# Kernel tuning notes

Hardware: AMD Instinct MI355X
Metric: run time of the kernel (lower is better)

## Reference

```python
import jax, jax.numpy as jnp
import numpy as np

N_VERT, D = 100000, 128
N_EDGE, K, R = 20000, 8, 4


def setup_inputs() -> dict:
    key = jax.random.key(0)
    ks = jax.random.split(key, 16)
    s = 0.05
    return {
        'feats': jax.random.normal(ks[0], (N_VERT, D), dtype=jnp.float32),
        'edge_members': jax.random.randint(ks[1], (N_EDGE, K), 0, N_VERT),
        'adj_members': jax.random.randint(ks[2], (N_EDGE, R, K), 0, N_VERT),
        'ids': jnp.arange(N_EDGE),
        'epoch': 10,
        # VertexConv params (Linear(d,1) each)
        'wq': jax.random.normal(ks[3], (D, 1)) * s, 'bq': jnp.zeros((1,)),
        'wk': jax.random.normal(ks[4], (D, 1)) * s, 'bk': jnp.zeros((1,)),
        'wv': jax.random.normal(ks[5], (D, 1)) * s, 'bv': jnp.zeros((1,)),
        # EdgeConv MLP: Linear(d, d//4) -> ReLU -> Linear(d//4, 1)
        'W1': jax.random.normal(ks[6], (D, D // 4)) * s, 'b1': jnp.zeros((D // 4,)),
        'W2': jax.random.normal(ks[7], (D // 4, 1)) * s, 'b2': jnp.zeros((1,)),
        # final classifier Linear(d, 2)
        'Wfc': jax.random.normal(ks[8], (D, 2)) * s, 'bfc': jnp.zeros((2,)),
    }


def _vertex_conv(feats, members, wq, bq, wk, bk, wv, bv):
    # members: [E, K] vertex indices; aggregates each hyperedge's vertices into one feature.
    f = feats[members]                         # [E,K,d] irregular gather
    q = f @ wq + bq                            # [E,K,1]
    k = f @ wk + bk                            # [E,K,1]
    v = f @ wv + bv                            # [E,K,1]
    # score[e,j,l] = q[e,j]*k[e,l]; original softmaxes over the K-1 "other" vertices (l != j)
    S = q * jnp.swapaxes(k, -1, -2)            # [E,K,K]
    S = jnp.where(jnp.eye(members.shape[-1], dtype=bool), -jnp.inf, S)
    a = jax.nn.softmax(S, axis=-1)             # [E,K,K]
    di = jnp.tanh(jnp.einsum('ejl,elo->ejo', a, v))  # [E,K,1] per-vertex scalar gate
    return (di * f).sum(axis=1)                # [E,d]


def reference(feats, edge_members, adj_members, ids, epoch,
              wq, bq, wk, bk, wv, bv, W1, b1, W2, b2, Wfc, bfc):
    n = edge_members.shape[0]
    # epoch >= wu_e(=0): hyperedge feature from edge_dict
    xn = _vertex_conv(feats, edge_members, wq, bq, wk, bk, wv, bv)   # [N,d]
    # epoch >= wu_a(=5): hyperedge features from each vertex's adjacent edges
    xe = _vertex_conv(feats, adj_members.reshape(n * R, K),
                      wq, bq, wk, bk, wv, bv).reshape(n, R, -1)       # [N,R,d]
    ft = jnp.concatenate([xn[:, None, :], xe], axis=1)                # [N,1+R,d]
    # EdgeConv: attention over the 1+R candidate hyperedge feats
    sc = jax.nn.relu(ft @ W1 + b1) @ W2 + b2                          # [N,1+R,1]
    a = jax.nn.softmax(sc, axis=1)
    h = (a * ft).sum(axis=1)                                          # [N,d]
    # dropout in eval mode (identity), then sigmoid(Linear(d,2))
    return jax.nn.sigmoid(h @ Wfc + bfc)                              # [N,2]
```

## Files before the change

kernel.cpp:

```cpp
#include <hip/hip_runtime.h>
#include <math.h>

#define KK 8
#define DD 128
#define RR 4
#define NG 5
#define HID 32
#define NC 40
#define NSLOT 48

typedef __attribute__((ext_vector_type(8))) short short8_t;
typedef __attribute__((ext_vector_type(4))) float f32x4_t;

__device__ __forceinline__ unsigned short f2bf(float x) {
    unsigned int u = __float_as_uint(x);
    unsigned int r = (u + 0x7FFFu + ((u >> 16) & 1u)) >> 16;
    return (unsigned short)r;
}
__device__ __forceinline__ float bf2f(unsigned short u) {
    return __uint_as_float((unsigned int)u << 16);
}

__global__ __launch_bounds__(256) void proj_mfma(
    const float* __restrict__ feats, int n_vert, int n_tg,
    const float* __restrict__ wq, const float* __restrict__ wk,
    const float* __restrict__ wv, const float* __restrict__ Wfc,
    const float* __restrict__ W1,
    const float* __restrict__ bq, const float* __restrict__ bk,
    const float* __restrict__ bv,
    unsigned short* __restrict__ proj)
{
    __shared__ short Bsh[12 * 64 * 8];

    const int t = threadIdx.x;
    const int wave = t >> 6, lane = t & 63;
    const int row = lane & 15;
    const int kg  = lane >> 4;

    #pragma unroll
    for (int q = 0; q < 3; ++q) {
        const int p = t + q * 256;
        const int ntks = p >> 6, plane = p & 63;
        const int nt = ntks >> 2, ks = ntks & 3;
        const int n  = nt * 16 + (plane & 15);
        const int k0 = ks * 32 + (plane >> 4) * 8;
        short8_t v;
        #pragma unroll
        for (int j = 0; j < 8; ++j) {
            const int k = k0 + j;
            float val;
            if      (n == 0) val = wq[k];
            else if (n == 1) val = wk[k];
            else if (n == 2) val = wv[k];
            else if (n == 3) val = Wfc[2 * k];
            else if (n == 4) val = Wfc[2 * k + 1];
            else if (n < 37) val = W1[k * HID + (n - 5)];
            else             val = 0.f;
            v[j] = (short)f2bf(val);
        }
        *(short8_t*)&Bsh[p * 8] = v;
    }

    const float bq0 = bq[0], bk0 = bk[0], bv0 = bv[0];
    __syncthreads();

    for (int tg = blockIdx.x; tg < n_tg; tg += gridDim.x) {
        const int mbase = (tg * 4 + wave) * 16;
        if (mbase >= n_vert) continue;

        long long arow = (long long)(mbase + row);
        if (arow >= n_vert) arow = n_vert - 1;
        const float* ar = &feats[arow * DD + kg * 8];
        float4 araw[8];
        #pragma unroll
        for (int ks = 0; ks < 4; ++ks) {
            araw[2 * ks]     = *(const float4*)&ar[ks * 32];
            araw[2 * ks + 1] = *(const float4*)&ar[ks * 32 + 4];
        }

        short8_t afrag[4];
        #pragma unroll
        for (int ks = 0; ks < 4; ++ks) {
            const float4 x0 = araw[2 * ks], x1 = araw[2 * ks + 1];
            short8_t a;
            a[0] = (short)f2bf(x0.x); a[1] = (short)f2bf(x0.y);
            a[2] = (short)f2bf(x0.z); a[3] = (short)f2bf(x0.w);
            a[4] = (short)f2bf(x1.x); a[5] = (short)f2bf(x1.y);
            a[6] = (short)f2bf(x1.z); a[7] = (short)f2bf(x1.w);
            afrag[ks] = a;
        }

        #pragma unroll
        for (int nt = 0; nt < 3; ++nt) {
            f32x4_t acc = {0.f, 0.f, 0.f, 0.f};
            #pragma unroll
            for (int ks = 0; ks < 4; ++ks) {
                const short8_t b = *(const short8_t*)&Bsh[((nt * 4 + ks) * 64 + lane) * 8];
                acc = __builtin_amdgcn_mfma_f32_16x16x32_bf16(afrag[ks], b, acc, 0, 0, 0);
            }
            const int col = nt * 16 + row;
            if (col < 37) {
                const int slot = (col < 5) ? col : (col + 3);
                float badd = 0.f;
                if      (col == 0) badd = bq0;
                else if (col == 1) badd = bk0;
                else if (col == 2) badd = bv0;
                #pragma unroll
                for (int r = 0; r < 4; ++r) {
                    const int vr = mbase + kg * 4 + r;
                    if (vr < n_vert)
                        proj[(long long)vr * NSLOT + slot] = f2bf(acc[r] + badd);
                }
            }
        }
    }
}

__global__ __launch_bounds__(256) void edge_fused(
    const int* __restrict__ edge_members,
    const int* __restrict__ adj_members,
    const unsigned short* __restrict__ proj,
    const float* __restrict__ b1, const float* __restrict__ W2,
    const float* __restrict__ b2, const float* __restrict__ bfc,
    float* __restrict__ out, int n_edge)
{
    __shared__ int   vidS[4][NG * KK];
    __shared__ float diS [4][NG * KK];
    __shared__ float ftfcS[4][NG][2];
    __shared__ float scS [4][NG];

    const int t = threadIdx.x;
    const int w = t >> 6;
    const int lane = t & 63;
    const int e = blockIdx.x * 4 + w;
    if (e >= n_edge) return;

    const int g = lane >> 3;
    const int j = lane & 7;
    const bool act = lane < NG * KK;

    int vid = 0;
    if (act) vid = (g == 0) ? edge_members[e * KK + j]
                            : adj_members[((e * RR) + (g - 1)) * KK + j];

    const uint4 qpu = *(const uint4*)&proj[(long long)vid * NSLOT];
    const float qv  = bf2f((unsigned short)(qpu.x & 0xFFFFu));
    const float kv  = bf2f((unsigned short)(qpu.x >> 16));
    const float vv  = bf2f((unsigned short)(qpu.y & 0xFFFFu));
    const float pf0 = bf2f((unsigned short)(qpu.y >> 16));
    const float pf1 = bf2f((unsigned short)(qpu.z & 0xFFFFu));

    float k8[KK], v8[KK];
    #pragma unroll
    for (int r = 0; r < KK; ++r) {
        k8[r] = __shfl(kv, (g << 3) + r);
        v8[r] = __shfl(vv, (g << 3) + r);
    }

    float mx = -1e30f;
    float s[KK];
    #pragma unroll
    for (int r = 0; r < KK; ++r) {
        s[r] = qv * k8[r];
        if (r != j) mx = fmaxf(mx, s[r]);
    }
    float den = 0.f, num = 0.f;
    #pragma unroll
    for (int r = 0; r < KK; ++r) {
        if (r == j) continue;
        const float ex = expf(s[r] - mx);
        den += ex;
        num += ex * v8[r];
    }
    const float di = tanhf(num / den);

    float px = di * pf0, py = di * pf1;
    #pragma unroll
    for (int mm = 4; mm >= 1; mm >>= 1) {
        px += __shfl_xor(px, mm);
        py += __shfl_xor(py, mm);
    }
    if (act) {
        vidS[w][lane] = vid;
        diS[w][lane]  = di;
        if (j == 0) { ftfcS[w][g][0] = px; ftfcS[w][g][1] = py; }
    }
    asm volatile("s_waitcnt lgkmcnt(0)" ::: "memory");

    const int m = lane & 31;
    const int h = lane >> 5;
    const float b1m = b1[m];
    const float w2m = W2[m];

    float dr2[3][KK];
    float pv2[3][KK];
    #pragma unroll
    for (int p = 0; p < 3; ++p) {
        const int grp = (p << 1) | h;
        if (grp < NG) {
            #pragma unroll
            for (int r = 0; r < KK; ++r) {
                const int vr = vidS[w][grp * KK + r];
                dr2[p][r] = diS[w][grp * KK + r];
                pv2[p][r] = bf2f(proj[(long long)vr * NSLOT + 8 + m]);
            }
        }
    }
    #pragma unroll
    for (int p = 0; p < 3; ++p) {
        const int grp = (p << 1) | h;
        if (grp < NG) {
            float acc = 0.f;
            #pragma unroll
            for (int r = 0; r < KK; ++r) acc += dr2[p][r] * pv2[p][r];
            float hid = fmaxf(acc + b1m, 0.f) * w2m;
            #pragma unroll
            for (int mm = 16; mm >= 1; mm >>= 1) hid += __shfl_xor(hid, mm);
            if (m == 0) scS[w][grp] = hid + b2[0];
        }
    }
    asm volatile("s_waitcnt lgkmcnt(0)" ::: "memory");

    if (lane < 2) {
        float sc0[NG];
        float m5 = -1e30f;
        #pragma unroll
        for (int gg = 0; gg < NG; ++gg) { sc0[gg] = scS[w][gg]; m5 = fmaxf(m5, sc0[gg]); }
        float ssum = 0.f;
        #pragma unroll
        for (int gg = 0; gg < NG; ++gg) { sc0[gg] = expf(sc0[gg] - m5); ssum += sc0[gg]; }
        const float inv = 1.f / ssum;
        float hc = 0.f;
        #pragma unroll
        for (int gg = 0; gg < NG; ++gg) hc += sc0[gg] * inv * ftfcS[w][gg][lane];
        const float z = hc + bfc[lane];
        out[e * 2 + lane] = 1.f / (1.f + expf(-z));
    }
}

extern "C" void kernel_launch(void* const* d_in, const int* in_sizes, int n_in,
                              void* d_out, int out_size, void* d_ws, size_t ws_size,
                              hipStream_t stream) {
    const float* feats        = (const float*)d_in[0];
    const int*   edge_members = (const int*)  d_in[1];
    const int*   adj_members  = (const int*)  d_in[2];
    const float* wq  = (const float*)d_in[5];
    const float* bq  = (const float*)d_in[6];
    const float* wk  = (const float*)d_in[7];
    const float* bk  = (const float*)d_in[8];
    const float* wv  = (const float*)d_in[9];
    const float* bv  = (const float*)d_in[10];
    const float* W1  = (const float*)d_in[11];
    const float* b1  = (const float*)d_in[12];
    const float* W2  = (const float*)d_in[13];
    const float* b2  = (const float*)d_in[14];
    const float* Wfc = (const float*)d_in[15];
    const float* bfc = (const float*)d_in[16];
    float* out = (float*)d_out;

    const int n_vert = in_sizes[0] / DD;
    const int n_edge = in_sizes[1] / KK;

    unsigned short* proj = (unsigned short*)d_ws;

    const int n_mtiles = (n_vert + 15) / 16;
    const int n_tg = (n_mtiles + 3) / 4;
    const int grid = (n_tg < 640) ? n_tg : 640;

    proj_mfma<<<grid, 256, 0, stream>>>(
        feats, n_vert, n_tg, wq, wk, wv, Wfc, W1, bq, bk, bv, proj);

    edge_fused<<<(n_edge + 3) / 4, 256, 0, stream>>>(
        edge_members, adj_members, proj, b1, W2, b2, bfc, out, n_edge);
}
```

Baseline: 41.97 us.

## Prefetch next feats tile in projection loop and drop LDS in edge kernel

The projection kernel now double-buffers its feature rows in registers, loading the next tile while converting and running MFMAs on the current one. The grid is resized so each block handles about two tiles. The edge kernel replaces shared-memory staging of vertex ids, gates and scores with wave shuffles, and issues the W1-hidden gathers early so they overlap the softmax math. This adds register pressure and extra shuffles in exchange for hiding global-load latency and removing LDS round trips.

```diff
diff --git a/kernel.cpp b/kernel.cpp
--- a/kernel.cpp
+++ b/kernel.cpp
@@ -6,7 +6,6 @@
 #define RR 4
 #define NG 5
 #define HID 32
-#define NC 40
 #define NSLOT 48
 
 typedef __attribute__((ext_vector_type(8))) short short8_t;
@@ -64,24 +63,42 @@
     const float bq0 = bq[0], bk0 = bk[0], bv0 = bv[0];
     __syncthreads();
 
-    for (int tg = blockIdx.x; tg < n_tg; tg += gridDim.x) {
-        const int mbase = (tg * 4 + wave) * 16;
-        if (mbase >= n_vert) continue;
-
-        long long arow = (long long)(mbase + row);
+    const int stride = gridDim.x;
+    int tg = blockIdx.x;
+    if (tg >= n_tg) return;
+
+    float4 cur[8];
+    {
+        long long arow = (long long)(tg * 4 + wave) * 16 + row;
         if (arow >= n_vert) arow = n_vert - 1;
         const float* ar = &feats[arow * DD + kg * 8];
-        float4 araw[8];
         #pragma unroll
         for (int ks = 0; ks < 4; ++ks) {
-            araw[2 * ks]     = *(const float4*)&ar[ks * 32];
-            araw[2 * ks + 1] = *(const float4*)&ar[ks * 32 + 4];
-        }
-
+            cur[2 * ks]     = *(const float4*)&ar[ks * 32];
+            cur[2 * ks + 1] = *(const float4*)&ar[ks * 32 + 4];
+        }
+    }
+
+    for (;;) {
+        const int tgn = tg + stride;
+        const bool more = (tgn < n_tg);
+        float4 nxt[8];
+        if (more) {
+            long long arow = (long long)(tgn * 4 + wave) * 16 + row;
+            if (arow >= n_vert) arow = n_vert - 1;
+            const float* ar = &feats[arow * DD + kg * 8];
+            #pragma unroll
+            for (int ks = 0; ks < 4; ++ks) {
+                nxt[2 * ks]     = *(const float4*)&ar[ks * 32];
+                nxt[2 * ks + 1] = *(const float4*)&ar[ks * 32 + 4];
+            }
+        }
+
+        const int mbase = (tg * 4 + wave) * 16;
         short8_t afrag[4];
         #pragma unroll
         for (int ks = 0; ks < 4; ++ks) {
-            const float4 x0 = araw[2 * ks], x1 = araw[2 * ks + 1];
+            const float4 x0 = cur[2 * ks], x1 = cur[2 * ks + 1];
             short8_t a;
             a[0] = (short)f2bf(x0.x); a[1] = (short)f2bf(x0.y);
             a[2] = (short)f2bf(x0.z); a[3] = (short)f2bf(x0.w);
@@ -89,7 +106,6 @@
             a[6] = (short)f2bf(x1.z); a[7] = (short)f2bf(x1.w);
             afrag[ks] = a;
         }
-
         #pragma unroll
         for (int nt = 0; nt < 3; ++nt) {
             f32x4_t acc = {0.f, 0.f, 0.f, 0.f};
@@ -113,6 +129,11 @@
                 }
             }
         }
+
+        if (!more) break;
+        #pragma unroll
+        for (int i = 0; i < 8; ++i) cur[i] = nxt[i];
+        tg = tgn;
     }
 }
 
@@ -124,11 +145,6 @@
     const float* __restrict__ b2, const float* __restrict__ bfc,
     float* __restrict__ out, int n_edge)
 {
-    __shared__ int   vidS[4][NG * KK];
-    __shared__ float diS [4][NG * KK];
-    __shared__ float ftfcS[4][NG][2];
-    __shared__ float scS [4][NG];
-
     const int t = threadIdx.x;
     const int w = t >> 6;
     const int lane = t & 63;
@@ -138,12 +154,27 @@
     const int g = lane >> 3;
     const int j = lane & 7;
     const bool act = lane < NG * KK;
+    const int m = lane & 31;
+    const int h = lane >> 5;
 
     int vid = 0;
     if (act) vid = (g == 0) ? edge_members[e * KK + j]
                             : adj_members[((e * RR) + (g - 1)) * KK + j];
 
     const uint4 qpu = *(const uint4*)&proj[(long long)vid * NSLOT];
+
+    float pv2[3][KK];
+    #pragma unroll
+    for (int p = 0; p < 3; ++p) {
+        const int grp = (p << 1) | h;
+        const int gsrc = (grp < NG) ? grp : 0;
+        #pragma unroll
+        for (int r = 0; r < KK; ++r) {
+            const int vr = __shfl(vid, gsrc * KK + r);
+            pv2[p][r] = bf2f(proj[(long long)vr * NSLOT + 8 + m]);
+        }
+    }
+
     const float qv  = bf2f((unsigned short)(qpu.x & 0xFFFFu));
     const float kv  = bf2f((unsigned short)(qpu.x >> 16));
     const float vv  = bf2f((unsigned short)(qpu.y & 0xFFFFu));
@@ -156,7 +187,6 @@
         k8[r] = __shfl(kv, (g << 3) + r);
         v8[r] = __shfl(vv, (g << 3) + r);
     }
-
     float mx = -1e30f;
     float s[KK];
     #pragma unroll
@@ -180,60 +210,46 @@
         px += __shfl_xor(px, mm);
         py += __shfl_xor(py, mm);
     }
-    if (act) {
-        vidS[w][lane] = vid;
-        diS[w][lane]  = di;
-        if (j == 0) { ftfcS[w][g][0] = px; ftfcS[w][g][1] = py; }
-    }
-    asm volatile("s_waitcnt lgkmcnt(0)" ::: "memory");
-
-    const int m = lane & 31;
-    const int h = lane >> 5;
+
     const float b1m = b1[m];
     const float w2m = W2[m];
-
-    float dr2[3][KK];
-    float pv2[3][KK];
+    float scr[3];
     #pragma unroll
     for (int p = 0; p < 3; ++p) {
         const int grp = (p << 1) | h;
-        if (grp < NG) {
-            #pragma unroll
-            for (int r = 0; r < KK; ++r) {
-                const int vr = vidS[w][grp * KK + r];
-                dr2[p][r] = diS[w][grp * KK + r];
-                pv2[p][r] = bf2f(proj[(long long)vr * NSLOT + 8 + m]);
-            }
-        }
-    }
-    #pragma unroll
-    for (int p = 0; p < 3; ++p) {
-        const int grp = (p << 1) | h;
-        if (grp < NG) {
-            float acc = 0.f;
-            #pragma unroll
-            for (int r = 0; r < KK; ++r) acc += dr2[p][r] * pv2[p][r];
-            float hid = fmaxf(acc + b1m, 0.f) * w2m;
-            #pragma unroll
-            for (int mm = 16; mm >= 1; mm >>= 1) hid += __shfl_xor(hid, mm);
-            if (m == 0) scS[w][grp] = hid + b2[0];
-        }
-    }
-    asm volatile("s_waitcnt lgkmcnt(0)" ::: "memory");
-
+        const int gsrc = (grp < NG) ? grp : 0;
+        float acc = 0.f;
+        #pragma unroll
+        for (int r = 0; r < KK; ++r)
+            acc += __shfl(di, gsrc * KK + r) * pv2[p][r];
+        float hid = fmaxf(acc + b1m, 0.f) * w2m;
+        #pragma unroll
+        for (int mm = 16; mm >= 1; mm >>= 1) hid += __shfl_xor(hid, mm);
+        scr[p] = hid;
+    }
+
+    float sc5[NG], fx5[NG], fy5[NG];
+    #pragma unroll
+    for (int gg = 0; gg < NG; ++gg) {
+        sc5[gg] = __shfl(scr[gg >> 1], (gg & 1) * 32) + b2[0];
+        fx5[gg] = __shfl(px, gg * 8);
+        fy5[gg] = __shfl(py, gg * 8);
+    }
+
+    float m5 = sc5[0];
+    #pragma unroll
+    for (int gg = 1; gg < NG; ++gg) m5 = fmaxf(m5, sc5[gg]);
+    float ssum = 0.f, h0 = 0.f, h1 = 0.f;
+    #pragma unroll
+    for (int gg = 0; gg < NG; ++gg) {
+        const float a = expf(sc5[gg] - m5);
+        ssum += a;
+        h0 += a * fx5[gg];
+        h1 += a * fy5[gg];
+    }
+    const float inv = 1.f / ssum;
     if (lane < 2) {
-        float sc0[NG];
-        float m5 = -1e30f;
-        #pragma unroll
-        for (int gg = 0; gg < NG; ++gg) { sc0[gg] = scS[w][gg]; m5 = fmaxf(m5, sc0[gg]); }
-        float ssum = 0.f;
-        #pragma unroll
-        for (int gg = 0; gg < NG; ++gg) { sc0[gg] = expf(sc0[gg] - m5); ssum += sc0[gg]; }
-        const float inv = 1.f / ssum;
-        float hc = 0.f;
-        #pragma unroll
-        for (int gg = 0; gg < NG; ++gg) hc += sc0[gg] * inv * ftfcS[w][gg][lane];
-        const float z = hc + bfc[lane];
+        const float z = ((lane == 0) ? h0 : h1) * inv + bfc[lane];
         out[e * 2 + lane] = 1.f / (1.f + expf(-z));
     }
 }
@@ -265,7 +281,7 @@
 
     const int n_mtiles = (n_vert + 15) / 16;
     const int n_tg = (n_mtiles + 3) / 4;
-    const int grid = (n_tg < 640) ? n_tg : 640;
+    const int grid = (n_tg + 1) / 2;
 
     proj_mfma<<<grid, 256, 0, stream>>>(
         feats, n_vert, n_tg, wq, wk, wv, Wfc, W1, bq, bk, bv, proj);
```

Result: slower. 48.31 us (+15.1%).
